# Performance work log

Hardware: AMD Instinct MI355X
Metric: run time of the kernel (lower is better)

The kernel has to match this reference:

```python
import jax, jax.numpy as jnp
import numpy as np

Q_WINDOW = 2  # matches init kwarg Q


def setup_inputs() -> dict:
    key = jax.random.key(0)
    k1, k2, k3 = jax.random.split(key, 3)
    B, M, D, C = 32, 2048, 1024, 5
    embeds_x = jax.random.normal(k1, (B, M, D), jnp.float32)
    embeds_y = jax.random.normal(k2, (B, C * D, 1), jnp.float32)
    # small scale on P keeps the bilinear logits in a sane softmax range
    P = jax.random.normal(k3, (D, C * D), jnp.float32) * 1e-3
    return {"embeds_x": embeds_x, "embeds_y": embeds_y, "P": P, "M": M}


def reference(embeds_x, embeds_y, P, M):
    # embeds_x: [B, M, D], embeds_y: [B, C*D, 1], P: [D, C*D]
    B, Mx, D = embeds_x.shape
    Q = Q_WINDOW

    # Sliding-window sums via cumsum (replaces the per-timestep Python loop).
    # Original torch code: x_bar[:, i, :] = sum(x[:, s:e, :]) / Q with
    # s = max(i-Q, 0), e = min(i+Q, M-1), slice end EXCLUSIVE, built from .data
    # (i.e. detached from autograd).
    cs = jnp.concatenate(
        [jnp.zeros((B, 1, D), embeds_x.dtype), jnp.cumsum(embeds_x, axis=1)], axis=1
    )  # [B, M+1, D]
    i = jnp.arange(M)
    s = jnp.clip(i - Q, 0, None)
    e = jnp.clip(i + Q, None, M - 1)
    x_bar = (cs[:, e, :] - cs[:, s, :]) / Q  # [B, M, D]
    x_bar = jax.lax.stop_gradient(x_bar)

    # Bilinear attention scores: a = P @ y, p = x @ a
    a = jnp.einsum('dk,bko->bdo', P, embeds_y)          # [B, D, 1]
    logits = jnp.einsum('bmd,bdo->bmo', embeds_x, a)    # [B, M, 1]
    # legacy F.softmax on [M, B, 1] -> dim 0, i.e. softmax over sequence M
    p = jax.nn.softmax(logits, axis=1)                  # [B, M, 1]

    # enc = (x_bar^T @ p).squeeze : weighted sum of smoothed embeddings
    enc = jnp.einsum('bmd,bmo->bd', x_bar, p)           # [B, D]
    return enc
```

## Files before the change

### kernel.cpp

```cpp
#include <hip/hip_runtime.h>

#define BB 32
#define MM 2048
#define DD 1024
#define KK 5120

#define R3 16
#define NCH 128

__global__ __launch_bounds__(256) void k_a(const float* __restrict__ P,
                                           const float* __restrict__ y,
                                           float* __restrict__ a) {
    const int d0 = blockIdx.x * 4;
    const int wave = threadIdx.x >> 6;
    const int lane = threadIdx.x & 63;
    const int b0 = wave * 8;

    float acc[4][8];
#pragma unroll
    for (int i = 0; i < 4; ++i)
#pragma unroll
        for (int j = 0; j < 8; ++j) acc[i][j] = 0.f;

    for (int i = 0; i < 20; ++i) {
        const int k4 = lane + i * 64;
        float4 pv[4], yv[8];
#pragma unroll
        for (int dd = 0; dd < 4; ++dd)
            pv[dd] = ((const float4*)(P + (size_t)(d0 + dd) * KK))[k4];
#pragma unroll
        for (int bb = 0; bb < 8; ++bb)
            yv[bb] = ((const float4*)(y + (size_t)(b0 + bb) * KK))[k4];
#pragma unroll
        for (int dd = 0; dd < 4; ++dd)
#pragma unroll
            for (int bb = 0; bb < 8; ++bb) {
                acc[dd][bb] = fmaf(pv[dd].x, yv[bb].x, acc[dd][bb]);
                acc[dd][bb] = fmaf(pv[dd].y, yv[bb].y, acc[dd][bb]);
                acc[dd][bb] = fmaf(pv[dd].z, yv[bb].z, acc[dd][bb]);
                acc[dd][bb] = fmaf(pv[dd].w, yv[bb].w, acc[dd][bb]);
            }
    }

#pragma unroll
    for (int dd = 0; dd < 4; ++dd)
#pragma unroll
        for (int bb = 0; bb < 8; ++bb) {
            float v = acc[dd][bb];
#pragma unroll
            for (int off = 32; off; off >>= 1) v += __shfl_xor(v, off, 64);
            if (lane == 0) a[(size_t)(b0 + bb) * DD + (d0 + dd)] = v;
        }
}

__global__ __launch_bounds__(256) void k_fused3(const float* __restrict__ x,
                                                const float* __restrict__ a,
                                                float* __restrict__ part,
                                                float* __restrict__ Spart) {
    const int w = threadIdx.x >> 6;
    const int lane = threadIdx.x & 63;
    const int g = blockIdx.x * 4 + w;
    const int b = g >> 7;
    const int chunk = g & (NCH - 1);
    const int j0 = chunk * R3;

    const float4* a4 = (const float4*)(a + (size_t)b * DD);
    const float4 av0 = a4[lane];
    const float4 av1 = a4[lane + 64];
    const float4 av2 = a4[lane + 128];
    const float4 av3 = a4[lane + 192];

    const float* xb = x + (size_t)b * MM * DD;
    const float4 fz = make_float4(0.f, 0.f, 0.f, 0.f);

    float4 xA0 = fz, xA1 = fz, xA2 = fz, xA3 = fz;
    float4 xB0 = fz, xB1 = fz, xB2 = fz, xB3 = fz;
    float4 xC0 = fz, xC1 = fz, xC2 = fz, xC3 = fz;
    float4 acc0 = fz, acc1 = fz, acc2 = fz, acc3 = fz;
    float e_m1 = 0.f, e_m2 = 0.f, e_m3 = 0.f;
    float se = 0.f;

#define STEP(IT, XL0, XL1, XL2, XL3, XC0, XC1, XC2, XC3)                     \
    {                                                                        \
        constexpr int it = (IT);                                             \
        const int m = j0 - 1 + it;                                           \
        bool vm = true;                                                      \
        if (it == 0) vm = (m >= 0);                                          \
        if (it >= 17) vm = (m < MM);                                         \
        if (vm) {                                                            \
            const float4* row4 = (const float4*)(xb + (size_t)m * DD);       \
            XL0 = row4[lane];                                                \
            XL1 = row4[lane + 64];                                           \
            XL2 = row4[lane + 128];                                          \
            XL3 = row4[lane + 192];                                          \
        } else {                                                             \
            XL0 = fz; XL1 = fz; XL2 = fz; XL3 = fz;                          \
        }                                                                    \
        float s_ = 0.f;                                                      \
        s_ = fmaf(XL0.x, av0.x, s_); s_ = fmaf(XL0.y, av0.y, s_);            \
        s_ = fmaf(XL0.z, av0.z, s_); s_ = fmaf(XL0.w, av0.w, s_);            \
        s_ = fmaf(XL1.x, av1.x, s_); s_ = fmaf(XL1.y, av1.y, s_);            \
        s_ = fmaf(XL1.z, av1.z, s_); s_ = fmaf(XL1.w, av1.w, s_);            \
        s_ = fmaf(XL2.x, av2.x, s_); s_ = fmaf(XL2.y, av2.y, s_);            \
        s_ = fmaf(XL2.z, av2.z, s_); s_ = fmaf(XL2.w, av2.w, s_);            \
        s_ = fmaf(XL3.x, av3.x, s_); s_ = fmaf(XL3.y, av3.y, s_);            \
        s_ = fmaf(XL3.z, av3.z, s_); s_ = fmaf(XL3.w, av3.w, s_);            \
        s_ += __shfl_xor(s_, 32, 64); s_ += __shfl_xor(s_, 16, 64);          \
        s_ += __shfl_xor(s_, 8, 64);  s_ += __shfl_xor(s_, 4, 64);           \
        s_ += __shfl_xor(s_, 2, 64);  s_ += __shfl_xor(s_, 1, 64);           \
        const float ecur = vm ? __expf(s_) : 0.f;                            \
        if (it >= 1 && it <= 16) se += ecur;                                 \
        if (it >= 3) {                                                       \
            const int j = j0 - 3 + it;                                       \
            float c = e_m3 + e_m2 + e_m1 + ecur;                             \
            if (j == MM - 1) c = 0.f;                                        \
            acc0.x = fmaf(c, XC0.x, acc0.x); acc0.y = fmaf(c, XC0.y, acc0.y);\
            acc0.z = fmaf(c, XC0.z, acc0.z); acc0.w = fmaf(c, XC0.w, acc0.w);\
            acc1.x = fmaf(c, XC1.x, acc1.x); acc1.y = fmaf(c, XC1.y, acc1.y);\
            acc1.z = fmaf(c, XC1.z, acc1.z); acc1.w = fmaf(c, XC1.w, acc1.w);\
            acc2.x = fmaf(c, XC2.x, acc2.x); acc2.y = fmaf(c, XC2.y, acc2.y);\
            acc2.z = fmaf(c, XC2.z, acc2.z); acc2.w = fmaf(c, XC2.w, acc2.w);\
            acc3.x = fmaf(c, XC3.x, acc3.x); acc3.y = fmaf(c, XC3.y, acc3.y);\
            acc3.z = fmaf(c, XC3.z, acc3.z); acc3.w = fmaf(c, XC3.w, acc3.w);\
        }                                                                    \
        e_m3 = e_m2; e_m2 = e_m1; e_m1 = ecur;                               \
    }

    STEP(0,  xA0, xA1, xA2, xA3,  xB0, xB1, xB2, xB3)
    STEP(1,  xB0, xB1, xB2, xB3,  xC0, xC1, xC2, xC3)
    STEP(2,  xC0, xC1, xC2, xC3,  xA0, xA1, xA2, xA3)
    STEP(3,  xA0, xA1, xA2, xA3,  xB0, xB1, xB2, xB3)
    STEP(4,  xB0, xB1, xB2, xB3,  xC0, xC1, xC2, xC3)
    STEP(5,  xC0, xC1, xC2, xC3,  xA0, xA1, xA2, xA3)
    STEP(6,  xA0, xA1, xA2, xA3,  xB0, xB1, xB2, xB3)
    STEP(7,  xB0, xB1, xB2, xB3,  xC0, xC1, xC2, xC3)
    STEP(8,  xC0, xC1, xC2, xC3,  xA0, xA1, xA2, xA3)
    STEP(9,  xA0, xA1, xA2, xA3,  xB0, xB1, xB2, xB3)
    STEP(10, xB0, xB1, xB2, xB3,  xC0, xC1, xC2, xC3)
    STEP(11, xC0, xC1, xC2, xC3,  xA0, xA1, xA2, xA3)
    STEP(12, xA0, xA1, xA2, xA3,  xB0, xB1, xB2, xB3)
    STEP(13, xB0, xB1, xB2, xB3,  xC0, xC1, xC2, xC3)
    STEP(14, xC0, xC1, xC2, xC3,  xA0, xA1, xA2, xA3)
    STEP(15, xA0, xA1, xA2, xA3,  xB0, xB1, xB2, xB3)
    STEP(16, xB0, xB1, xB2, xB3,  xC0, xC1, xC2, xC3)
    STEP(17, xC0, xC1, xC2, xC3,  xA0, xA1, xA2, xA3)
    STEP(18, xA0, xA1, xA2, xA3,  xB0, xB1, xB2, xB3)
#undef STEP

    float4* p4 = (float4*)part + (size_t)(b * NCH + chunk) * 256;
    p4[lane] = acc0;
    p4[lane + 64] = acc1;
    p4[lane + 128] = acc2;
    p4[lane + 192] = acc3;
    if (lane == 0) Spart[b * NCH + chunk] = se;
}

__global__ __launch_bounds__(256) void k_combine3(const float* __restrict__ part,
                                                  const float* __restrict__ Spart,
                                                  float* __restrict__ out) {
    const int b = blockIdx.y;
    const int sl = blockIdx.x;
    const int t = threadIdx.x;
    const int col = t & 31;
    const int grp = t >> 5;

    __shared__ float Ssh;
    __shared__ float4 red[8][32];

    if (t < 64) {
        float s = Spart[b * NCH + t] + Spart[b * NCH + 64 + t];
#pragma unroll
        for (int off = 32; off; off >>= 1) s += __shfl_xor(s, off, 64);
        if (t == 0) Ssh = s;
    }

    float4 acc = make_float4(0.f, 0.f, 0.f, 0.f);
    const float4* p4 = (const float4*)part + (size_t)b * NCH * 256 + sl * 32 + col;
    for (int c = grp; c < NCH; c += 8) {
        const float4 v = p4[(size_t)c * 256];
        acc.x += v.x; acc.y += v.y; acc.z += v.z; acc.w += v.w;
    }
    red[grp][col] = acc;
    __syncthreads();

    if (t < 32) {
        float4 s = red[0][t];
#pragma unroll
        for (int g2 = 1; g2 < 8; ++g2) {
            const float4 v = red[g2][t];
            s.x += v.x; s.y += v.y; s.z += v.z; s.w += v.w;
        }
        const float invS = 0.5f / Ssh;
        ((float4*)(out + (size_t)b * DD))[sl * 32 + t] =
            make_float4(s.x * invS, s.y * invS, s.z * invS, s.w * invS);
    }
}

__global__ __launch_bounds__(256) void k_logits(const float* __restrict__ x,
                                                const float* __restrict__ a,
                                                float* __restrict__ logits) {
    const int b = blockIdx.y;
    const int wave = threadIdx.x >> 6;
    const int lane = threadIdx.x & 63;
    const int m = blockIdx.x * 8 + wave * 2;
    const float* ab = a + (size_t)b * DD;
    const float* row0 = x + ((size_t)b * MM + m) * DD;
    const float* row1 = row0 + DD;
    float s0 = 0.f, s1 = 0.f;
#pragma unroll
    for (int q = 0; q < 4; ++q) {
        const int d = lane * 4 + q * 256;
        const float4 av = *(const float4*)(ab + d);
        const float4 x0 = *(const float4*)(row0 + d);
        const float4 x1 = *(const float4*)(row1 + d);
        s0 = fmaf(x0.x, av.x, s0); s0 = fmaf(x0.y, av.y, s0);
        s0 = fmaf(x0.z, av.z, s0); s0 = fmaf(x0.w, av.w, s0);
        s1 = fmaf(x1.x, av.x, s1); s1 = fmaf(x1.y, av.y, s1);
        s1 = fmaf(x1.z, av.z, s1); s1 = fmaf(x1.w, av.w, s1);
    }
#pragma unroll
    for (int off = 32; off; off >>= 1) {
        s0 += __shfl_xor(s0, off, 64);
        s1 += __shfl_xor(s1, off, 64);
    }
    if (lane == 0) {
        logits[(size_t)b * MM + m] = s0;
        logits[(size_t)b * MM + m + 1] = s1;
    }
}

__global__ __launch_bounds__(256) void k_softmax_w(const float* __restrict__ logits,
                                                   float* __restrict__ w) {
    const int b = blockIdx.x;
    __shared__ float p[MM];
    __shared__ float red[8];
    const int t = threadIdx.x;
    const int lane = t & 63, wave = t >> 6;
    float mx = -INFINITY;
    for (int m = t; m < MM; m += 256) {
        const float v = logits[(size_t)b * MM + m];
        p[m] = v;
        mx = fmaxf(mx, v);
    }
#pragma unroll
    for (int off = 32; off; off >>= 1) mx = fmaxf(mx, __shfl_xor(mx, off, 64));
    if (lane == 0) red[wave] = mx;
    __syncthreads();
    mx = fmaxf(fmaxf(red[0], red[1]), fmaxf(red[2], red[3]));
    float s = 0.f;
    for (int m = t; m < MM; m += 256) {
        const float e = __expf(p[m] - mx);
        p[m] = e;
        s += e;
    }
#pragma unroll
    for (int off = 32; off; off >>= 1) s += __shfl_xor(s, off, 64);
    if (lane == 0) red[4 + wave] = s;
    __syncthreads();
    s = red[4] + red[5] + red[6] + red[7];
    const float inv = 0.5f / s;
    for (int j = t; j < MM; j += 256) {
        float wv;
        if (j == MM - 1) wv = 0.f;
        else {
            float acc = p[j];
            if (j >= 1) acc += p[j - 1];
            if (j + 1 <= MM - 1) acc += p[j + 1];
            if (j + 2 <= MM - 1) acc += p[j + 2];
            wv = acc * inv;
        }
        w[(size_t)b * MM + j] = wv;
    }
}

__global__ void k_zero(float* __restrict__ out) {
    out[blockIdx.x * 256 + threadIdx.x] = 0.f;
}

__global__ __launch_bounds__(256) void k_enc(const float* __restrict__ x,
                                             const float* __restrict__ w,
                                             float* __restrict__ out) {
    const int b = (BB - 1) - blockIdx.y;
    const int chunk = 31 - blockIdx.x;
    const int j0 = chunk * (MM / 32);
    const int d = threadIdx.x * 4;
    float4 acc0 = {0.f, 0.f, 0.f, 0.f};
    float4 acc1 = {0.f, 0.f, 0.f, 0.f};
    const float* xb = x + (size_t)b * MM * DD + d;
    const float* wb = w + (size_t)b * MM;
    for (int j = j0 + (MM / 32) - 1; j >= j0; j -= 2) {
        const float w0 = wb[j];
        const float w1 = wb[j - 1];
        const float4 x0 = *(const float4*)(xb + (size_t)j * DD);
        const float4 x1 = *(const float4*)(xb + (size_t)(j - 1) * DD);
        acc0.x = fmaf(w0, x0.x, acc0.x); acc0.y = fmaf(w0, x0.y, acc0.y);
        acc0.z = fmaf(w0, x0.z, acc0.z); acc0.w = fmaf(w0, x0.w, acc0.w);
        acc1.x = fmaf(w1, x1.x, acc1.x); acc1.y = fmaf(w1, x1.y, acc1.y);
        acc1.z = fmaf(w1, x1.z, acc1.z); acc1.w = fmaf(w1, x1.w, acc1.w);
    }
    float* o = out + (size_t)b * DD + d;
    atomicAdd(o + 0, acc0.x + acc1.x);
    atomicAdd(o + 1, acc0.y + acc1.y);
    atomicAdd(o + 2, acc0.z + acc1.z);
    atomicAdd(o + 3, acc0.w + acc1.w);
}

extern "C" void kernel_launch(void* const* d_in, const int* in_sizes, int n_in,
                              void* d_out, int out_size, void* d_ws, size_t ws_size,
                              hipStream_t stream) {
    (void)in_sizes; (void)n_in; (void)out_size;
    const float* x = (const float*)d_in[0];
    const float* y = (const float*)d_in[1];
    const float* P = (const float*)d_in[2];
    float* out = (float*)d_out;

    float* ws = (float*)d_ws;
    float* a = ws;
    const size_t part_f = (size_t)BB * NCH * DD;
    const size_t need = (32768 + part_f + BB * NCH) * sizeof(float);

    k_a<<<dim3(DD / 4), dim3(256), 0, stream>>>(P, y, a);

    if (ws_size >= need) {
        float* part = ws + 32768;
        float* Spart = part + part_f;
        k_fused3<<<dim3(BB * NCH / 4), dim3(256), 0, stream>>>(x, a, part, Spart);
        k_combine3<<<dim3(8, BB), dim3(256), 0, stream>>>(part, Spart, out);
    } else {
        float* logits = ws + 32768;
        float* w = ws + 32768 + 65536;
        k_logits<<<dim3(MM / 8, BB), dim3(256), 0, stream>>>(x, a, logits);
        k_softmax_w<<<dim3(BB), dim3(256), 0, stream>>>(logits, w);
        k_zero<<<dim3((BB * DD) / 256), dim3(256), 0, stream>>>(out);
        k_enc<<<dim3(32, BB), dim3(256), 0, stream>>>(x, w, out);
    }
}
```

Baseline: 92.66 us.

## Prefetch x rows one step ahead with 4-slot rotation and swizzle block order

The fused logits/softmax/weighted-sum kernel now issues each row load one step before the row's dot product is used, rotating through four register slots instead of three. This lets global loads overlap the shuffle reduction and exp work. Block indices are also swizzled so concurrently scheduled blocks touch different batches and chunks, and launch bounds now request 4 blocks per CU. The cost is one more row of float4 registers per lane and one extra pipeline step, which may raise register pressure.

```diff
diff --git a/kernel.cpp b/kernel.cpp
--- a/kernel.cpp
+++ b/kernel.cpp
@@ -53,13 +53,15 @@
         }
 }
 
-__global__ __launch_bounds__(256) void k_fused3(const float* __restrict__ x,
-                                                const float* __restrict__ a,
-                                                float* __restrict__ part,
-                                                float* __restrict__ Spart) {
+__global__ __launch_bounds__(256, 4) void k_fused5(const float* __restrict__ x,
+                                                   const float* __restrict__ a,
+                                                   float* __restrict__ part,
+                                                   float* __restrict__ Spart) {
     const int w = threadIdx.x >> 6;
     const int lane = threadIdx.x & 63;
-    const int g = blockIdx.x * 4 + w;
+    const int bid = blockIdx.x;
+    const int swz = (bid & 7) * 128 + (bid >> 3);
+    const int g = swz * 4 + w;
     const int b = g >> 7;
     const int chunk = g & (NCH - 1);
     const int j0 = chunk * R3;
@@ -73,78 +75,79 @@
     const float* xb = x + (size_t)b * MM * DD;
     const float4 fz = make_float4(0.f, 0.f, 0.f, 0.f);
 
-    float4 xA0 = fz, xA1 = fz, xA2 = fz, xA3 = fz;
-    float4 xB0 = fz, xB1 = fz, xB2 = fz, xB3 = fz;
-    float4 xC0 = fz, xC1 = fz, xC2 = fz, xC3 = fz;
+    float4 S00 = fz, S01 = fz, S02 = fz, S03 = fz;
+    float4 S10 = fz, S11 = fz, S12 = fz, S13 = fz;
+    float4 S20 = fz, S21 = fz, S22 = fz, S23 = fz;
+    float4 S30 = fz, S31 = fz, S32 = fz, S33 = fz;
     float4 acc0 = fz, acc1 = fz, acc2 = fz, acc3 = fz;
-    float e_m1 = 0.f, e_m2 = 0.f, e_m3 = 0.f;
+    float e1 = 0.f, e2 = 0.f, e3 = 0.f;
     float se = 0.f;
 
-#define STEP(IT, XL0, XL1, XL2, XL3, XC0, XC1, XC2, XC3)                     \
+#define STEP(IT, L0, L1, L2, L3, D0, D1, D2, D3, W0, W1, W2, W3)             \
     {                                                                        \
         constexpr int it = (IT);                                             \
-        const int m = j0 - 1 + it;                                           \
-        bool vm = true;                                                      \
-        if (it == 0) vm = (m >= 0);                                          \
-        if (it >= 17) vm = (m < MM);                                         \
-        if (vm) {                                                            \
-            const float4* row4 = (const float4*)(xb + (size_t)m * DD);       \
-            XL0 = row4[lane];                                                \
-            XL1 = row4[lane + 64];                                           \
-            XL2 = row4[lane + 128];                                          \
-            XL3 = row4[lane + 192];                                          \
-        } else {                                                             \
-            XL0 = fz; XL1 = fz; XL2 = fz; XL3 = fz;                          \
+        if (it <= 18) {                                                      \
+            const int ml = j0 - 1 + it;                                      \
+            if (ml >= 0 && ml < MM) {                                        \
+                const float4* r4_ = (const float4*)(xb + (size_t)ml * DD);   \
+                L0 = r4_[lane];       L1 = r4_[lane + 64];                   \
+                L2 = r4_[lane + 128]; L3 = r4_[lane + 192];                  \
+            } else { L0 = fz; L1 = fz; L2 = fz; L3 = fz; }                   \
         }                                                                    \
-        float s_ = 0.f;                                                      \
-        s_ = fmaf(XL0.x, av0.x, s_); s_ = fmaf(XL0.y, av0.y, s_);            \
-        s_ = fmaf(XL0.z, av0.z, s_); s_ = fmaf(XL0.w, av0.w, s_);            \
-        s_ = fmaf(XL1.x, av1.x, s_); s_ = fmaf(XL1.y, av1.y, s_);            \
-        s_ = fmaf(XL1.z, av1.z, s_); s_ = fmaf(XL1.w, av1.w, s_);            \
-        s_ = fmaf(XL2.x, av2.x, s_); s_ = fmaf(XL2.y, av2.y, s_);            \
-        s_ = fmaf(XL2.z, av2.z, s_); s_ = fmaf(XL2.w, av2.w, s_);            \
-        s_ = fmaf(XL3.x, av3.x, s_); s_ = fmaf(XL3.y, av3.y, s_);            \
-        s_ = fmaf(XL3.z, av3.z, s_); s_ = fmaf(XL3.w, av3.w, s_);            \
-        s_ += __shfl_xor(s_, 32, 64); s_ += __shfl_xor(s_, 16, 64);          \
-        s_ += __shfl_xor(s_, 8, 64);  s_ += __shfl_xor(s_, 4, 64);           \
-        s_ += __shfl_xor(s_, 2, 64);  s_ += __shfl_xor(s_, 1, 64);           \
-        const float ecur = vm ? __expf(s_) : 0.f;                            \
-        if (it >= 1 && it <= 16) se += ecur;                                 \
-        if (it >= 3) {                                                       \
-            const int j = j0 - 3 + it;                                       \
-            float c = e_m3 + e_m2 + e_m1 + ecur;                             \
-            if (j == MM - 1) c = 0.f;                                        \
-            acc0.x = fmaf(c, XC0.x, acc0.x); acc0.y = fmaf(c, XC0.y, acc0.y);\
-            acc0.z = fmaf(c, XC0.z, acc0.z); acc0.w = fmaf(c, XC0.w, acc0.w);\
-            acc1.x = fmaf(c, XC1.x, acc1.x); acc1.y = fmaf(c, XC1.y, acc1.y);\
-            acc1.z = fmaf(c, XC1.z, acc1.z); acc1.w = fmaf(c, XC1.w, acc1.w);\
-            acc2.x = fmaf(c, XC2.x, acc2.x); acc2.y = fmaf(c, XC2.y, acc2.y);\
-            acc2.z = fmaf(c, XC2.z, acc2.z); acc2.w = fmaf(c, XC2.w, acc2.w);\
-            acc3.x = fmaf(c, XC3.x, acc3.x); acc3.y = fmaf(c, XC3.y, acc3.y);\
-            acc3.z = fmaf(c, XC3.z, acc3.z); acc3.w = fmaf(c, XC3.w, acc3.w);\
+        if (it >= 1) {                                                       \
+            const int md = j0 - 2 + it;                                      \
+            const bool vd = (md >= 0) && (md < MM);                          \
+            float s_ = 0.f;                                                  \
+            s_ = fmaf(D0.x, av0.x, s_); s_ = fmaf(D0.y, av0.y, s_);          \
+            s_ = fmaf(D0.z, av0.z, s_); s_ = fmaf(D0.w, av0.w, s_);          \
+            s_ = fmaf(D1.x, av1.x, s_); s_ = fmaf(D1.y, av1.y, s_);          \
+            s_ = fmaf(D1.z, av1.z, s_); s_ = fmaf(D1.w, av1.w, s_);          \
+            s_ = fmaf(D2.x, av2.x, s_); s_ = fmaf(D2.y, av2.y, s_);          \
+            s_ = fmaf(D2.z, av2.z, s_); s_ = fmaf(D2.w, av2.w, s_);          \
+            s_ = fmaf(D3.x, av3.x, s_); s_ = fmaf(D3.y, av3.y, s_);          \
+            s_ = fmaf(D3.z, av3.z, s_); s_ = fmaf(D3.w, av3.w, s_);          \
+            s_ += __shfl_xor(s_, 32, 64); s_ += __shfl_xor(s_, 16, 64);      \
+            s_ += __shfl_xor(s_, 8, 64);  s_ += __shfl_xor(s_, 4, 64);       \
+            s_ += __shfl_xor(s_, 2, 64);  s_ += __shfl_xor(s_, 1, 64);       \
+            const float ecur = vd ? __expf(s_) : 0.f;                        \
+            if (it >= 2 && it <= 17) se += ecur;                             \
+            if (it >= 4) {                                                   \
+                const int j = j0 - 4 + it;                                   \
+                float c = e3 + e2 + e1 + ecur;                               \
+                if (j == MM - 1) c = 0.f;                                    \
+                acc0.x = fmaf(c, W0.x, acc0.x); acc0.y = fmaf(c, W0.y, acc0.y); \
+                acc0.z = fmaf(c, W0.z, acc0.z); acc0.w = fmaf(c, W0.w, acc0.w); \
+                acc1.x = fmaf(c, W1.x, acc1.x); acc1.y = fmaf(c, W1.y, acc1.y); \
+                acc1.z = fmaf(c, W1.z, acc1.z); acc1.w = fmaf(c, W1.w, acc1.w); \
+                acc2.x = fmaf(c, W2.x, acc2.x); acc2.y = fmaf(c, W2.y, acc2.y); \
+                acc2.z = fmaf(c, W2.z, acc2.z); acc2.w = fmaf(c, W2.w, acc2.w); \
+                acc3.x = fmaf(c, W3.x, acc3.x); acc3.y = fmaf(c, W3.y, acc3.y); \
+                acc3.z = fmaf(c, W3.z, acc3.z); acc3.w = fmaf(c, W3.w, acc3.w); \
+            }                                                                \
+            e3 = e2; e2 = e1; e1 = ecur;                                     \
         }                                                                    \
-        e_m3 = e_m2; e_m2 = e_m1; e_m1 = ecur;                               \
-    }
-
-    STEP(0,  xA0, xA1, xA2, xA3,  xB0, xB1, xB2, xB3)
-    STEP(1,  xB0, xB1, xB2, xB3,  xC0, xC1, xC2, xC3)
-    STEP(2,  xC0, xC1, xC2, xC3,  xA0, xA1, xA2, xA3)
-    STEP(3,  xA0, xA1, xA2, xA3,  xB0, xB1, xB2, xB3)
-    STEP(4,  xB0, xB1, xB2, xB3,  xC0, xC1, xC2, xC3)
-    STEP(5,  xC0, xC1, xC2, xC3,  xA0, xA1, xA2, xA3)
-    STEP(6,  xA0, xA1, xA2, xA3,  xB0, xB1, xB2, xB3)
-    STEP(7,  xB0, xB1, xB2, xB3,  xC0, xC1, xC2, xC3)
-    STEP(8,  xC0, xC1, xC2, xC3,  xA0, xA1, xA2, xA3)
-    STEP(9,  xA0, xA1, xA2, xA3,  xB0, xB1, xB2, xB3)
-    STEP(10, xB0, xB1, xB2, xB3,  xC0, xC1, xC2, xC3)
-    STEP(11, xC0, xC1, xC2, xC3,  xA0, xA1, xA2, xA3)
-    STEP(12, xA0, xA1, xA2, xA3,  xB0, xB1, xB2, xB3)
-    STEP(13, xB0, xB1, xB2, xB3,  xC0, xC1, xC2, xC3)
-    STEP(14, xC0, xC1, xC2, xC3,  xA0, xA1, xA2, xA3)
-    STEP(15, xA0, xA1, xA2, xA3,  xB0, xB1, xB2, xB3)
-    STEP(16, xB0, xB1, xB2, xB3,  xC0, xC1, xC2, xC3)
-    STEP(17, xC0, xC1, xC2, xC3,  xA0, xA1, xA2, xA3)
-    STEP(18, xA0, xA1, xA2, xA3,  xB0, xB1, xB2, xB3)
+    }
+
+    STEP(0,  S00,S01,S02,S03, S30,S31,S32,S33, S10,S11,S12,S13)
+    STEP(1,  S10,S11,S12,S13, S00,S01,S02,S03, S20,S21,S22,S23)
+    STEP(2,  S20,S21,S22,S23, S10,S11,S12,S13, S30,S31,S32,S33)
+    STEP(3,  S30,S31,S32,S33, S20,S21,S22,S23, S00,S01,S02,S03)
+    STEP(4,  S00,S01,S02,S03, S30,S31,S32,S33, S10,S11,S12,S13)
+    STEP(5,  S10,S11,S12,S13, S00,S01,S02,S03, S20,S21,S22,S23)
+    STEP(6,  S20,S21,S22,S23, S10,S11,S12,S13, S30,S31,S32,S33)
+    STEP(7,  S30,S31,S32,S33, S20,S21,S22,S23, S00,S01,S02,S03)
+    STEP(8,  S00,S01,S02,S03, S30,S31,S32,S33, S10,S11,S12,S13)
+    STEP(9,  S10,S11,S12,S13, S00,S01,S02,S03, S20,S21,S22,S23)
+    STEP(10, S20,S21,S22,S23, S10,S11,S12,S13, S30,S31,S32,S33)
+    STEP(11, S30,S31,S32,S33, S20,S21,S22,S23, S00,S01,S02,S03)
+    STEP(12, S00,S01,S02,S03, S30,S31,S32,S33, S10,S11,S12,S13)
+    STEP(13, S10,S11,S12,S13, S00,S01,S02,S03, S20,S21,S22,S23)
+    STEP(14, S20,S21,S22,S23, S10,S11,S12,S13, S30,S31,S32,S33)
+    STEP(15, S30,S31,S32,S33, S20,S21,S22,S23, S00,S01,S02,S03)
+    STEP(16, S00,S01,S02,S03, S30,S31,S32,S33, S10,S11,S12,S13)
+    STEP(17, S10,S11,S12,S13, S00,S01,S02,S03, S20,S21,S22,S23)
+    STEP(18, S20,S21,S22,S23, S10,S11,S12,S13, S30,S31,S32,S33)
+    STEP(19, S30,S31,S32,S33, S20,S21,S22,S23, S00,S01,S02,S03)
 #undef STEP
 
     float4* p4 = (float4*)part + (size_t)(b * NCH + chunk) * 256;
@@ -324,7 +327,7 @@
     if (ws_size >= need) {
         float* part = ws + 32768;
         float* Spart = part + part_f;
-        k_fused3<<<dim3(BB * NCH / 4), dim3(256), 0, stream>>>(x, a, part, Spart);
+        k_fused5<<<dim3(BB * NCH / 4), dim3(256), 0, stream>>>(x, a, part, Spart);
         k_combine3<<<dim3(8, BB), dim3(256), 0, stream>>>(part, Spart, out);
     } else {
         float* logits = ws + 32768;
```

Measured after the change: 229.6 us. 148% more time.
